# Performance work log

Hardware: AMD Instinct MI355X
Metric: run time of the kernel (lower is better)

The kernel has to match this reference:

```python
import jax, jax.numpy as jnp
import numpy as np

N_NODES = 50000
N_EDGES = 800000
ORIG_FEA = 92
NBR_FEA = 41
HID = 64
N_CONV = 3
BN_EPS = 1e-5


def setup_inputs() -> dict:
    key = jax.random.key(0)
    ks = jax.random.split(key, 16)
    s = 0.05
    inp = {
        "x": jax.random.normal(ks[0], (N_NODES, ORIG_FEA), dtype=jnp.float32),
        "edge_attr": jax.random.normal(ks[1], (N_EDGES, NBR_FEA), dtype=jnp.float32),
        "edge_index": jax.random.randint(ks[2], (2, N_EDGES), 0, N_NODES, dtype=jnp.int64),
        # embedding1 / embedding2
        "W1": jax.random.normal(ks[3], (ORIG_FEA, HID), dtype=jnp.float32) * s,
        "b1": jnp.zeros((HID,), dtype=jnp.float32),
        "W2": jax.random.normal(ks[4], (NBR_FEA, HID), dtype=jnp.float32) * s,
        "b2": jnp.zeros((HID,), dtype=jnp.float32),
        # CGConv lin_f / lin_s per layer, stacked [n_conv, 3*HID, HID]
        "Wf": jax.random.normal(ks[5], (N_CONV, 3 * HID, HID), dtype=jnp.float32) * s,
        "bf": jnp.zeros((N_CONV, HID), dtype=jnp.float32),
        "Ws": jax.random.normal(ks[6], (N_CONV, 3 * HID, HID), dtype=jnp.float32) * s,
        "bs": jnp.zeros((N_CONV, HID), dtype=jnp.float32),
        # BatchNorm1d per layer (training mode: batch statistics)
        "gamma": jnp.ones((N_CONV, HID), dtype=jnp.float32),
        "beta": jnp.zeros((N_CONV, HID), dtype=jnp.float32),
    }
    return inp


def _cgconv(x, e, src, tgt, Wf, bf, Ws, bs):
    # z_ij = [x_i (target), x_j (source), e_ij]  -> [E, 3H]
    z = jnp.concatenate([x[tgt], x[src], e], axis=-1)
    gate = jax.nn.sigmoid(z @ Wf + bf)
    core = jax.nn.softplus(z @ Ws + bs)
    msg = gate * core  # [E, H]
    agg = jax.ops.segment_sum(msg, tgt, num_segments=x.shape[0])
    return x + agg  # residual


def _batchnorm(x, gamma, beta):
    mean = jnp.mean(x, axis=0)
    var = jnp.mean(jnp.square(x - mean), axis=0)  # biased var (torch BN training)
    return (x - mean) * jax.lax.rsqrt(var + BN_EPS) * gamma + beta


def reference(x, edge_attr, edge_index, W1, b1, W2, b2, Wf, bf, Ws, bs, gamma, beta):
    src, tgt = edge_index[0], edge_index[1]
    h = x @ W1 + b1                 # embedding1: [N, H]
    e = edge_attr @ W2 + b2         # embedding2: [E, H]
    for i in range(N_CONV):
        h = _cgconv(h, e, src, tgt, Wf[i], bf[i], Ws[i], bs[i])
        h = _batchnorm(h, gamma[i], beta[i])
        if i < N_CONV - 1:
            h = jax.nn.relu(h)
        # drop_ratio = 0 -> dropout is identity
    return h
```

## Files before the change

kernel.cpp:

```cpp
#include <hip/hip_runtime.h>
#include <cmath>

#define NNODES 50000
#define NEDGES 800000
#define ORIG_FEA 92
#define NBR_FEA 41
#define HID 64
#define BN_EPS 1e-5f

typedef __attribute__((ext_vector_type(8))) short short8;
typedef __attribute__((ext_vector_type(4))) float f32x4;
typedef unsigned short ushort;
typedef unsigned int uint;

static __device__ __forceinline__ ushort f2bf(float f) {
    uint u = __float_as_uint(f);
    uint r = u + 0x7fffu + ((u >> 16) & 1u);
    return (ushort)(r >> 16);
}

__global__ void prep(const float* __restrict__ W2, const float* __restrict__ b2,
                     const float* __restrict__ Wf, const float* __restrict__ bf,
                     const float* __restrict__ Ws, const float* __restrict__ bs,
                     ushort* __restrict__ Bpack, ushort* __restrict__ Tpack,
                     float* __restrict__ bcf, float* __restrict__ bcs,
                     float* __restrict__ stats) {
    if (blockIdx.x == 6) {
        for (int i = threadIdx.x; i < 3 * 128; i += blockDim.x) stats[i] = 0.f;
        return;
    }
    int layer = blockIdx.x >> 1;
    int fs = blockIdx.x & 1;
    const float* Wbig = (fs ? Ws : Wf) + layer * 192 * HID;
    const float* We = Wbig + 128 * HID;
    const float* bvec = (fs ? bs : bf) + layer * HID;
    float* bc = (fs ? bcs : bcf) + layer * HID;
    ushort* Bp = Bpack + layer * 16384 + fs * 8192;
    ushort* Tp = Tpack + layer * 8192 + fs * 4096;

    for (int idx = threadIdx.x; idx < 8192; idx += blockDim.x) {
        int j = idx & 7;
        int lane = (idx >> 3) & 63;
        int ck = (idx >> 9) & 3;
        int tt = (idx >> 11) & 3;
        int k = ck * 32 + ((lane >> 4) * 8) + j;
        int col = tt * 16 + (lane & 15);
        float v = 0.f;
        if (k < 64) v = Wbig[(64 + k) * HID + col];
        else if (k < 64 + NBR_FEA) {
            int r = k - 64;
            float a = 0.f;
            for (int m = 0; m < HID; ++m) a += W2[r * HID + m] * We[m * HID + col];
            v = a;
        }
        Bp[(tt * 4 + ck) * 512 + lane * 8 + j] = f2bf(v);
    }
    for (int idx = threadIdx.x; idx < 4096; idx += blockDim.x) {
        int j = idx & 7;
        int lane = (idx >> 3) & 63;
        int ck = (idx >> 9) & 1;
        int t = (idx >> 10) & 3;
        int k = ck * 32 + ((lane >> 4) * 8) + j;
        int col = t * 16 + (lane & 15);
        Tp[(t * 2 + ck) * 512 + lane * 8 + j] = f2bf(Wbig[k * HID + col]);
    }
    for (int c0 = threadIdx.x; c0 < HID; c0 += blockDim.x) {
        float a = bvec[c0];
        for (int m = 0; m < HID; ++m) a += b2[m] * We[m * HID + c0];
        bc[c0] = a;
    }
}

__global__ void k_hist(const int* __restrict__ eidx, int* __restrict__ deg) {
    int e = blockIdx.x * blockDim.x + threadIdx.x;
    if (e < NEDGES) atomicAdd(&deg[eidx[NEDGES + e]], 1);
}

__global__ void k_blocksum(const int* __restrict__ deg, int* __restrict__ bsum) {
    __shared__ int sh[256];
    int i = blockIdx.x * 256 + threadIdx.x;
    sh[threadIdx.x] = (i < NNODES) ? deg[i] : 0;
    __syncthreads();
    for (int s = 128; s > 0; s >>= 1) {
        if (threadIdx.x < s) sh[threadIdx.x] += sh[threadIdx.x + s];
        __syncthreads();
    }
    if (threadIdx.x == 0) bsum[blockIdx.x] = sh[0];
}

__global__ void k_scanbase(const int* __restrict__ bsum, int* __restrict__ bbase,
                           int* __restrict__ rowptr) {
    __shared__ int sh[256];
    int t = threadIdx.x;
    int v = (t < 196) ? bsum[t] : 0;
    sh[t] = v;
    __syncthreads();
    for (int s = 1; s < 256; s <<= 1) {
        int add = (t >= s) ? sh[t - s] : 0;
        __syncthreads();
        sh[t] += add;
        __syncthreads();
    }
    if (t < 196) bbase[t] = sh[t] - v;
    if (t == 0) rowptr[NNODES] = NEDGES;
}

__global__ void k_writerow(const int* __restrict__ deg, const int* __restrict__ bbase,
                           int* __restrict__ rowptr, int* __restrict__ cursor) {
    __shared__ int sh[256];
    int t = threadIdx.x;
    int i = blockIdx.x * 256 + t;
    int v = (i < NNODES) ? deg[i] : 0;
    sh[t] = v;
    __syncthreads();
    for (int s = 1; s < 256; s <<= 1) {
        int add = (t >= s) ? sh[t - s] : 0;
        __syncthreads();
        sh[t] += add;
        __syncthreads();
    }
    if (i < NNODES) {
        int e = bbase[blockIdx.x] + sh[t] - v;
        rowptr[i] = e;
        cursor[i] = e;
    }
}

__global__ void k_scatterA(const int* __restrict__ eidx, int* __restrict__ cursor,
                           int* __restrict__ eorig, int* __restrict__ srcs) {
    int e = blockIdx.x * blockDim.x + threadIdx.x;
    if (e < NEDGES) {
        int tgt = eidx[NEDGES + e];
        int pos = atomicAdd(&cursor[tgt], 1);
        eorig[pos] = e;
        srcs[pos] = eidx[e];
    }
}

__global__ void k_scatterB(const float* __restrict__ ea, const int* __restrict__ eorig,
                           ushort* __restrict__ eab_s) {
    long idx = (long)blockIdx.x * blockDim.x + threadIdx.x;
    if (idx >= (long)NEDGES * 8) return;
    int pos = (int)(idx >> 3);
    int j = (int)(idx & 7);
    int e = eorig[pos];
    uint w[4];
    #pragma unroll
    for (int m = 0; m < 4; ++m) {
        int k0 = j * 8 + m * 2, k1 = k0 + 1;
        uint u0 = (k0 < NBR_FEA) ? (uint)f2bf(ea[(long)e * NBR_FEA + k0]) : 0u;
        uint u1 = (k1 < NBR_FEA) ? (uint)f2bf(ea[(long)e * NBR_FEA + k1]) : 0u;
        w[m] = u0 | (u1 << 16);
    }
    uint4 o; o.x = w[0]; o.y = w[1]; o.z = w[2]; o.w = w[3];
    *(uint4*)(eab_s + (long)pos * 64 + j * 8) = o;
}

__global__ __launch_bounds__(256) void embed(const float* __restrict__ x,
                                             const float* __restrict__ W1,
                                             const float* __restrict__ b1,
                                             float* __restrict__ h,
                                             ushort* __restrict__ h_bf) {
    int lane = threadIdx.x & 63;
    int wid = (blockIdx.x * blockDim.x + threadIdx.x) >> 6;
    int nw = (gridDim.x * blockDim.x) >> 6;
    float b1v = b1[lane];
    for (int n = wid; n < NNODES; n += nw) {
        const float* xr = x + (long)n * ORIG_FEA;
        float xa = xr[lane];
        float xb = (lane < ORIG_FEA - 64) ? xr[64 + lane] : 0.f;
        float a0 = b1v, a1 = 0.f, a2 = 0.f, a3 = 0.f;
        #pragma unroll
        for (int k = 0; k < 64; k += 4) {
            a0 = fmaf(__shfl(xa, k, 64),     W1[k * HID + lane], a0);
            a1 = fmaf(__shfl(xa, k + 1, 64), W1[(k + 1) * HID + lane], a1);
            a2 = fmaf(__shfl(xa, k + 2, 64), W1[(k + 2) * HID + lane], a2);
            a3 = fmaf(__shfl(xa, k + 3, 64), W1[(k + 3) * HID + lane], a3);
        }
        #pragma unroll
        for (int k = 0; k < ORIG_FEA - 64; k += 4) {
            a0 = fmaf(__shfl(xb, k, 64),     W1[(64 + k) * HID + lane], a0);
            a1 = fmaf(__shfl(xb, k + 1, 64), W1[(65 + k) * HID + lane], a1);
            a2 = fmaf(__shfl(xb, k + 2, 64), W1[(66 + k) * HID + lane], a2);
            a3 = fmaf(__shfl(xb, k + 3, 64), W1[(67 + k) * HID + lane], a3);
        }
        float acc = (a0 + a1) + (a2 + a3);
        h[(long)n * HID + lane] = acc;
        h_bf[(long)n * HID + lane] = f2bf(acc);
    }
}

__global__ __launch_bounds__(256) void proj_mfma(
    const ushort* __restrict__ h_bf, const ushort* __restrict__ Tpack_l,
    const float* __restrict__ bcf_l, const float* __restrict__ bcs_l,
    float* __restrict__ Ttgt) {
    int lane = threadIdx.x & 63;
    int cc = lane & 15;
    int g = lane >> 4;
    short8 Bf[4][2], Bs[4][2];
    #pragma unroll
    for (int t = 0; t < 4; ++t)
        #pragma unroll
        for (int ck = 0; ck < 2; ++ck) {
            Bf[t][ck] = *(const short8*)(Tpack_l + (t * 2 + ck) * 512 + lane * 8);
            Bs[t][ck] = *(const short8*)(Tpack_l + 4096 + (t * 2 + ck) * 512 + lane * 8);
        }
    float bfv[4], bsv[4];
    #pragma unroll
    for (int t = 0; t < 4; ++t) {
        bfv[t] = bcf_l[t * 16 + cc];
        bsv[t] = bcs_l[t * 16 + cc];
    }
    int wid = (blockIdx.x * blockDim.x + threadIdx.x) >> 6;
    int nw = (gridDim.x * blockDim.x) >> 6;
    for (int nb = wid; nb < NNODES / 16; nb += nw) {
        long base = (long)nb * 16;
        long row = base + cc;
        short8 A0 = *(const short8*)(h_bf + row * 64 + g * 8);
        short8 A1 = *(const short8*)(h_bf + row * 64 + 32 + g * 8);
        f32x4 accf[4], accs[4];
        f32x4 z4 = {0.f, 0.f, 0.f, 0.f};
        #pragma unroll
        for (int t = 0; t < 4; ++t) {
            accf[t] = __builtin_amdgcn_mfma_f32_16x16x32_bf16(A0, Bf[t][0], z4, 0, 0, 0);
            accs[t] = __builtin_amdgcn_mfma_f32_16x16x32_bf16(A0, Bs[t][0], z4, 0, 0, 0);
        }
        #pragma unroll
        for (int t = 0; t < 4; ++t) {
            accf[t] = __builtin_amdgcn_mfma_f32_16x16x32_bf16(A1, Bf[t][1], accf[t], 0, 0, 0);
            accs[t] = __builtin_amdgcn_mfma_f32_16x16x32_bf16(A1, Bs[t][1], accs[t], 0, 0, 0);
        }
        #pragma unroll
        for (int r = 0; r < 4; ++r) {
            long node = base + g * 4 + r;
            f32x4 vf = {accf[0][r] + bfv[0], accf[1][r] + bfv[1],
                        accf[2][r] + bfv[2], accf[3][r] + bfv[3]};
            f32x4 vs = {accs[0][r] + bsv[0], accs[1][r] + bsv[1],
                        accs[2][r] + bsv[2], accs[3][r] + bsv[3]};
            *(f32x4*)(Ttgt + node * 128 + cc * 4) = vf;
            *(f32x4*)(Ttgt + node * 128 + 64 + cc * 4) = vs;
        }
    }
}

__global__ __launch_bounds__(256, 2) void edge_kernel(
    const ushort* __restrict__ eab_s, const int* __restrict__ srcs,
    const int* __restrict__ rowptr, const ushort* __restrict__ h_bf,
    const float* __restrict__ h, const float* __restrict__ Ttgt,
    const ushort* __restrict__ Bpack, float* __restrict__ agg,
    float* __restrict__ stats) {
    int lane = threadIdx.x & 63;
    int q = lane >> 4;
    int c = lane & 15;
    int wid = (blockIdx.x * blockDim.x + threadIdx.x) >> 6;
    int nw = (gridDim.x * blockDim.x) >> 6;

    short8 B[8][4];
    #pragma unroll
    for (int t = 0; t < 8; ++t)
        #pragma unroll
        for (int ck = 0; ck < 4; ++ck)
            B[t][ck] = *(const short8*)(Bpack + ((t * 4 + ck) * 512 + lane * 8));

    float st1 = 0.f, st2 = 0.f;
    int tn = wid;
    int r0 = 0, r1 = 0, svAll = 0;
    short8 A0, A1, A2, A3;
    if (tn < NNODES) {
        r0 = rowptr[tn]; r1 = rowptr[tn + 1];
        int e = r0 + lane; if (e > NEDGES - 1) e = NEDGES - 1;
        svAll = srcs[e];
        int sv = __shfl(svAll, c, 64);
        int ei = r0 + c; if (ei > NEDGES - 1) ei = NEDGES - 1;
        const short8* hrow = (const short8*)(h_bf + (long)sv * 64);
        const short8* erow = (const short8*)(eab_s + (long)ei * 64);
        A0 = hrow[q]; A1 = hrow[4 + q]; A2 = erow[q]; A3 = erow[4 + q];
    }

    while (tn < NNODES) {
        int tn2 = tn + nw;
        int r0n = 0, r1n = 0;
        if (tn2 < NNODES) { r0n = rowptr[tn2]; r1n = rowptr[tn2 + 1]; }
        f32x4 tf = *(const f32x4*)(Ttgt + (long)tn * 128 + 4 * c);
        f32x4 ts = *(const f32x4*)(Ttgt + (long)tn * 128 + 64 + 4 * c);
        int d = r1 - r0;
        int nch = (d + 15) >> 4;
        float vs0 = 0.f, vs1 = 0.f, vs2 = 0.f, vs3 = 0.f;

        if (nch == 0) {
            int e = r0n + lane; if (e > NEDGES - 1) e = NEDGES - 1;
            svAll = srcs[e];
            int sv = __shfl(svAll, c, 64);
            int ei = r0n + c; if (ei > NEDGES - 1) ei = NEDGES - 1;
            const short8* hrow = (const short8*)(h_bf + (long)sv * 64);
            const short8* erow = (const short8*)(eab_s + (long)ei * 64);
            A0 = hrow[q]; A1 = hrow[4 + q]; A2 = erow[q]; A3 = erow[4 + q];
        } else {
            for (int ci = 0; ci < nch; ++ci) {
                int sv, ei;
                int nidx = ci + 1;
                if (nidx < nch) {
                    if ((nidx & 3) == 0) {
                        int e = r0 + nidx * 16 + lane;
                        if (e > NEDGES - 1) e = NEDGES - 1;
                        svAll = srcs[e];
                    }
                    sv = __shfl(svAll, ((nidx & 3) << 4) + c, 64);
                    ei = r0 + nidx * 16 + c;
                    if (ei > NEDGES - 1) ei = NEDGES - 1;
                } else {
                    int e = r0n + lane; if (e > NEDGES - 1) e = NEDGES - 1;
                    svAll = srcs[e];
                    sv = __shfl(svAll, c, 64);
                    ei = r0n + c; if (ei > NEDGES - 1) ei = NEDGES - 1;
                }
                const short8* hrow = (const short8*)(h_bf + (long)sv * 64);
                const short8* erow = (const short8*)(eab_s + (long)ei * 64);
                short8 N0 = hrow[q], N1 = hrow[4 + q];
                short8 N2 = erow[q], N3 = erow[4 + q];

                f32x4 accf[4], accs[4];
                f32x4 z4 = {0.f, 0.f, 0.f, 0.f};
                #pragma unroll
                for (int t = 0; t < 4; ++t) {
                    accf[t] = __builtin_amdgcn_mfma_f32_16x16x32_bf16(A0, B[t][0], z4, 0, 0, 0);
                    accs[t] = __builtin_amdgcn_mfma_f32_16x16x32_bf16(A0, B[t + 4][0], z4, 0, 0, 0);
                }
                #pragma unroll
                for (int t = 0; t < 4; ++t) {
                    accf[t] = __builtin_amdgcn_mfma_f32_16x16x32_bf16(A1, B[t][1], accf[t], 0, 0, 0);
                    accs[t] = __builtin_amdgcn_mfma_f32_16x16x32_bf16(A1, B[t + 4][1], accs[t], 0, 0, 0);
                }
                #pragma unroll
                for (int t = 0; t < 4; ++t) {
                    accf[t] = __builtin_amdgcn_mfma_f32_16x16x32_bf16(A2, B[t][2], accf[t], 0, 0, 0);
                    accs[t] = __builtin_amdgcn_mfma_f32_16x16x32_bf16(A2, B[t + 4][2], accs[t], 0, 0, 0);
                }
                #pragma unroll
                for (int t = 0; t < 4; ++t) {
                    accf[t] = __builtin_amdgcn_mfma_f32_16x16x32_bf16(A3, B[t][3], accf[t], 0, 0, 0);
                    accs[t] = __builtin_amdgcn_mfma_f32_16x16x32_bf16(A3, B[t + 4][3], accs[t], 0, 0, 0);
                }

                int base = ci * 16 + q * 4;
                #pragma unroll
                for (int r = 0; r < 4; ++r) {
                    bool valid = (base + r) < d;
                    #pragma unroll
                    for (int t = 0; t < 4; ++t) {
                        float f = accf[t][r] + tf[t];
                        float s = accs[t][r] + ts[t];
                        float g = __builtin_amdgcn_rcpf(1.f + __expf(-f));
                        float sp = fmaxf(s, 0.f) + __logf(1.f + __expf(-fabsf(s)));
                        float msg = valid ? g * sp : 0.f;
                        if (t == 0) vs0 += msg;
                        else if (t == 1) vs1 += msg;
                        else if (t == 2) vs2 += msg;
                        else vs3 += msg;
                    }
                }
                A0 = N0; A1 = N1; A2 = N2; A3 = N3;
            }
        }
        vs0 += __shfl_xor(vs0, 16, 64); vs0 += __shfl_xor(vs0, 32, 64);
        vs1 += __shfl_xor(vs1, 16, 64); vs1 += __shfl_xor(vs1, 32, 64);
        vs2 += __shfl_xor(vs2, 16, 64); vs2 += __shfl_xor(vs2, 32, 64);
        vs3 += __shfl_xor(vs3, 16, 64); vs3 += __shfl_xor(vs3, 32, 64);
        float out = (q == 0) ? vs0 : (q == 1) ? vs1 : (q == 2) ? vs2 : vs3;
        agg[(long)tn * 64 + lane] = out;
        float v = h[(long)tn * 64 + lane] + out;
        st1 += v;
        st2 = fmaf(v, v, st2);

        tn = tn2; r0 = r0n; r1 = r1n;
    }

    __shared__ float ls[4][64], lq[4][64];
    int w = threadIdx.x >> 6;
    ls[w][lane] = st1; lq[w][lane] = st2;
    __syncthreads();
    if (threadIdx.x < 64) {
        float t1 = ls[0][lane] + ls[1][lane] + ls[2][lane] + ls[3][lane];
        float t2 = lq[0][lane] + lq[1][lane] + lq[2][lane] + lq[3][lane];
        atomicAdd(&stats[lane], t1);
        atomicAdd(&stats[64 + lane], t2);
    }
}

__global__ __launch_bounds__(256) void bn_apply(
    float* __restrict__ h, const float* __restrict__ agg,
    const float* __restrict__ stats, const float* __restrict__ gamma,
    const float* __restrict__ beta, ushort* __restrict__ h_bf, int relu) {
    int tid = blockIdx.x * blockDim.x + threadIdx.x;
    int nth = gridDim.x * blockDim.x;
    const float invn = 1.f / (float)NNODES;
    int cb = (tid & 15) * 4;
    f32x4 sc, sh;
    #pragma unroll
    for (int j = 0; j < 4; ++j) {
        float m = stats[cb + j] * invn;
        float v = stats[64 + cb + j] * invn - m * m;
        float s = rsqrtf(v + BN_EPS) * gamma[cb + j];
        sc[j] = s;
        sh[j] = beta[cb + j] - m * s;
    }
    for (long i = tid; i < (long)NNODES * 16; i += nth) {
        f32x4 v = ((const f32x4*)h)[i];
        f32x4 a = ((const f32x4*)agg)[i];
        f32x4 y;
        #pragma unroll
        for (int j = 0; j < 4; ++j) {
            float t = (v[j] + a[j]) * sc[j] + sh[j];
            y[j] = relu ? fmaxf(t, 0.f) : t;
        }
        ((f32x4*)h)[i] = y;
        uint lo = (uint)f2bf(y[0]) | ((uint)f2bf(y[1]) << 16);
        uint hi = (uint)f2bf(y[2]) | ((uint)f2bf(y[3]) << 16);
        uint2 o; o.x = lo; o.y = hi;
        *(uint2*)(h_bf + i * 4) = o;
    }
}

extern "C" void kernel_launch(void* const* d_in, const int* in_sizes, int n_in,
                              void* d_out, int out_size, void* d_ws, size_t ws_size,
                              hipStream_t stream) {
    const float* x    = (const float*)d_in[0];
    const float* ea   = (const float*)d_in[1];
    const int*   eidx = (const int*)d_in[2];
    const float* W1   = (const float*)d_in[3];
    const float* b1   = (const float*)d_in[4];
    const float* W2   = (const float*)d_in[5];
    const float* b2   = (const float*)d_in[6];
    const float* Wf   = (const float*)d_in[7];
    const float* bf   = (const float*)d_in[8];
    const float* Ws   = (const float*)d_in[9];
    const float* bs   = (const float*)d_in[10];
    const float* gamma= (const float*)d_in[11];
    const float* beta = (const float*)d_in[12];
    float* h = (float*)d_out;

    char* wb = (char*)d_ws;
    auto align = [&]() { wb = (char*)(((size_t)wb + 255) & ~(size_t)255); };
    ushort* Bpack = (ushort*)wb;  wb += 3 * 8 * 4 * 512 * sizeof(ushort); align();
    ushort* Tpack = (ushort*)wb;  wb += 3 * 2 * 4 * 2 * 512 * sizeof(ushort); align();
    float* bcf   = (float*)wb;    wb += 3 * HID * sizeof(float);
    float* bcs   = (float*)wb;    wb += 3 * HID * sizeof(float);
    float* stats = (float*)wb;    wb += 3 * 2 * HID * sizeof(float); align();
    int* deg     = (int*)wb;      wb += NNODES * sizeof(int);
    int* rowptr  = (int*)wb;      wb += (NNODES + 1) * sizeof(int);
    int* cursor  = (int*)wb;      wb += NNODES * sizeof(int);
    int* bsum    = (int*)wb;      wb += 256 * sizeof(int);
    int* bbase   = (int*)wb;      wb += 256 * sizeof(int); align();
    int* eorig   = (int*)wb;      wb += NEDGES * sizeof(int);
    int* srcs    = (int*)wb;      wb += NEDGES * sizeof(int);
    align();
    float* Ttgt  = (float*)wb;    wb += (size_t)NNODES * 128 * sizeof(float);
    float* agg   = (float*)wb;    wb += (size_t)NNODES * HID * sizeof(float);
    ushort* h_bf = (ushort*)wb;   wb += (size_t)NNODES * HID * sizeof(ushort);
    ushort* eab_s= (ushort*)wb;   wb += (size_t)NEDGES * 64 * sizeof(ushort);

    prep<<<7, 256, 0, stream>>>(W2, b2, Wf, bf, Ws, bs, Bpack, Tpack, bcf, bcs, stats);

    hipMemsetAsync(deg, 0, NNODES * sizeof(int), stream);
    k_hist<<<(NEDGES + 255) / 256, 256, 0, stream>>>(eidx, deg);
    k_blocksum<<<196, 256, 0, stream>>>(deg, bsum);
    k_scanbase<<<1, 256, 0, stream>>>(bsum, bbase, rowptr);
    k_writerow<<<196, 256, 0, stream>>>(deg, bbase, rowptr, cursor);
    k_scatterA<<<(NEDGES + 255) / 256, 256, 0, stream>>>(eidx, cursor, eorig, srcs);
    k_scatterB<<<(NEDGES * 8 + 255) / 256, 256, 0, stream>>>(ea, eorig, eab_s);

    embed<<<2048, 256, 0, stream>>>(x, W1, b1, h, h_bf);
    proj_mfma<<<1024, 256, 0, stream>>>(h_bf, Tpack, bcf, bcs, Ttgt);

    for (int i = 0; i < 3; ++i) {
        edge_kernel<<<2048, 256, 0, stream>>>(eab_s, srcs, rowptr, h_bf, h, Ttgt,
                                              Bpack + i * 16384, agg, stats + i * 128);
        bn_apply<<<2048, 256, 0, stream>>>(h, agg, stats + i * 128, gamma + i * HID,
                                           beta + i * HID, h_bf, (i < 2) ? 1 : 0);
        if (i < 2)
            proj_mfma<<<1024, 256, 0, stream>>>(h_bf, Tpack + (i + 1) * 8192,
                                                bcf + (i + 1) * HID, bcs + (i + 1) * HID,
                                                Ttgt);
    }
}
```

Measured before the change: 853.3 us.

## Fuse BN with next-layer projection, merge embed with edge scatter, shrink edge rows

Several changes land together. BatchNorm+ReLU is fused with the next layer's target projection, so h_bf no longer makes a round trip through memory. The node embedding is merged into the edge-attribute scatter kernel, and that scatter now works per edge through a position array instead of per sorted slot through eorig. Stored edge rows shrink from 64 to 48 bf16 columns, and the padded tail loads are zeroed. The deg memset moves into prep, and s_setprio is added around the MFMA block. Together these aim to cut launch count and memory traffic, with a risk of tiling or layout bugs in the fused code paths.

Result: faster. 832.0 us (-2.5%).

```diff
diff --git a/kernel.cpp b/kernel.cpp
--- a/kernel.cpp
+++ b/kernel.cpp
@@ -7,6 +7,8 @@
 #define NBR_FEA 41
 #define HID 64
 #define BN_EPS 1e-5f
+#define ECOLS 48
+#define EMB_BLOCKS 1024
 
 typedef __attribute__((ext_vector_type(8))) short short8;
 typedef __attribute__((ext_vector_type(4))) float f32x4;
@@ -24,7 +26,12 @@
                      const float* __restrict__ Ws, const float* __restrict__ bs,
                      ushort* __restrict__ Bpack, ushort* __restrict__ Tpack,
                      float* __restrict__ bcf, float* __restrict__ bcs,
-                     float* __restrict__ stats) {
+                     float* __restrict__ stats, int* __restrict__ deg) {
+    if (blockIdx.x >= 7) {
+        int i = (blockIdx.x - 7) * 256 + threadIdx.x;
+        if (i < NNODES) deg[i] = 0;
+        return;
+    }
     if (blockIdx.x == 6) {
         for (int i = threadIdx.x; i < 3 * 128; i += blockDim.x) stats[i] = 0.f;
         return;
@@ -127,23 +134,57 @@
 }
 
 __global__ void k_scatterA(const int* __restrict__ eidx, int* __restrict__ cursor,
-                           int* __restrict__ eorig, int* __restrict__ srcs) {
+                           int* __restrict__ posarr, int* __restrict__ srcs) {
     int e = blockIdx.x * blockDim.x + threadIdx.x;
     if (e < NEDGES) {
         int tgt = eidx[NEDGES + e];
         int pos = atomicAdd(&cursor[tgt], 1);
-        eorig[pos] = e;
+        posarr[e] = pos;
         srcs[pos] = eidx[e];
     }
 }
 
-__global__ void k_scatterB(const float* __restrict__ ea, const int* __restrict__ eorig,
-                           ushort* __restrict__ eab_s) {
-    long idx = (long)blockIdx.x * blockDim.x + threadIdx.x;
-    if (idx >= (long)NEDGES * 8) return;
-    int pos = (int)(idx >> 3);
-    int j = (int)(idx & 7);
-    int e = eorig[pos];
+__global__ __launch_bounds__(256) void scatterB_embed(
+    const float* __restrict__ ea, const int* __restrict__ posarr,
+    ushort* __restrict__ eab_s,
+    const float* __restrict__ x, const float* __restrict__ W1,
+    const float* __restrict__ b1, float* __restrict__ h,
+    ushort* __restrict__ h_bf) {
+    if (blockIdx.x < EMB_BLOCKS) {
+        int lane = threadIdx.x & 63;
+        int wid = (blockIdx.x * blockDim.x + threadIdx.x) >> 6;
+        int nw = (EMB_BLOCKS * 256) >> 6;
+        float b1v = b1[lane];
+        for (int n = wid; n < NNODES; n += nw) {
+            const float* xr = x + (long)n * ORIG_FEA;
+            float xa = xr[lane];
+            float xb = (lane < ORIG_FEA - 64) ? xr[64 + lane] : 0.f;
+            float a0 = b1v, a1 = 0.f, a2 = 0.f, a3 = 0.f;
+            #pragma unroll
+            for (int k = 0; k < 64; k += 4) {
+                a0 = fmaf(__shfl(xa, k, 64),     W1[k * HID + lane], a0);
+                a1 = fmaf(__shfl(xa, k + 1, 64), W1[(k + 1) * HID + lane], a1);
+                a2 = fmaf(__shfl(xa, k + 2, 64), W1[(k + 2) * HID + lane], a2);
+                a3 = fmaf(__shfl(xa, k + 3, 64), W1[(k + 3) * HID + lane], a3);
+            }
+            #pragma unroll
+            for (int k = 0; k < ORIG_FEA - 64; k += 4) {
+                a0 = fmaf(__shfl(xb, k, 64),     W1[(64 + k) * HID + lane], a0);
+                a1 = fmaf(__shfl(xb, k + 1, 64), W1[(65 + k) * HID + lane], a1);
+                a2 = fmaf(__shfl(xb, k + 2, 64), W1[(66 + k) * HID + lane], a2);
+                a3 = fmaf(__shfl(xb, k + 3, 64), W1[(67 + k) * HID + lane], a3);
+            }
+            float acc = (a0 + a1) + (a2 + a3);
+            h[(long)n * HID + lane] = acc;
+            h_bf[(long)n * HID + lane] = f2bf(acc);
+        }
+        return;
+    }
+    long idx = (long)(blockIdx.x - EMB_BLOCKS) * blockDim.x + threadIdx.x;
+    if (idx >= (long)NEDGES * 6) return;
+    int e = (int)(idx / 6);
+    int j = (int)(idx - (long)e * 6);
+    int p = posarr[e];
     uint w[4];
     #pragma unroll
     for (int m = 0; m < 4; ++m) {
@@ -153,41 +194,7 @@
         w[m] = u0 | (u1 << 16);
     }
     uint4 o; o.x = w[0]; o.y = w[1]; o.z = w[2]; o.w = w[3];
-    *(uint4*)(eab_s + (long)pos * 64 + j * 8) = o;
-}
-
-__global__ __launch_bounds__(256) void embed(const float* __restrict__ x,
-                                             const float* __restrict__ W1,
-                                             const float* __restrict__ b1,
-                                             float* __restrict__ h,
-                                             ushort* __restrict__ h_bf) {
-    int lane = threadIdx.x & 63;
-    int wid = (blockIdx.x * blockDim.x + threadIdx.x) >> 6;
-    int nw = (gridDim.x * blockDim.x) >> 6;
-    float b1v = b1[lane];
-    for (int n = wid; n < NNODES; n += nw) {
-        const float* xr = x + (long)n * ORIG_FEA;
-        float xa = xr[lane];
-        float xb = (lane < ORIG_FEA - 64) ? xr[64 + lane] : 0.f;
-        float a0 = b1v, a1 = 0.f, a2 = 0.f, a3 = 0.f;
-        #pragma unroll
-        for (int k = 0; k < 64; k += 4) {
-            a0 = fmaf(__shfl(xa, k, 64),     W1[k * HID + lane], a0);
-            a1 = fmaf(__shfl(xa, k + 1, 64), W1[(k + 1) * HID + lane], a1);
-            a2 = fmaf(__shfl(xa, k + 2, 64), W1[(k + 2) * HID + lane], a2);
-            a3 = fmaf(__shfl(xa, k + 3, 64), W1[(k + 3) * HID + lane], a3);
-        }
-        #pragma unroll
-        for (int k = 0; k < ORIG_FEA - 64; k += 4) {
-            a0 = fmaf(__shfl(xb, k, 64),     W1[(64 + k) * HID + lane], a0);
-            a1 = fmaf(__shfl(xb, k + 1, 64), W1[(65 + k) * HID + lane], a1);
-            a2 = fmaf(__shfl(xb, k + 2, 64), W1[(66 + k) * HID + lane], a2);
-            a3 = fmaf(__shfl(xb, k + 3, 64), W1[(67 + k) * HID + lane], a3);
-        }
-        float acc = (a0 + a1) + (a2 + a3);
-        h[(long)n * HID + lane] = acc;
-        h_bf[(long)n * HID + lane] = f2bf(acc);
-    }
+    *(uint4*)(eab_s + (long)p * ECOLS + j * 8) = o;
 }
 
 __global__ __launch_bounds__(256) void proj_mfma(
@@ -254,6 +261,7 @@
     int c = lane & 15;
     int wid = (blockIdx.x * blockDim.x + threadIdx.x) >> 6;
     int nw = (gridDim.x * blockDim.x) >> 6;
+    const short8 z8 = {0, 0, 0, 0, 0, 0, 0, 0};
 
     short8 B[8][4];
     #pragma unroll
@@ -273,8 +281,11 @@
         int sv = __shfl(svAll, c, 64);
         int ei = r0 + c; if (ei > NEDGES - 1) ei = NEDGES - 1;
         const short8* hrow = (const short8*)(h_bf + (long)sv * 64);
-        const short8* erow = (const short8*)(eab_s + (long)ei * 64);
-        A0 = hrow[q]; A1 = hrow[4 + q]; A2 = erow[q]; A3 = erow[4 + q];
+        const ushort* erow = eab_s + (long)ei * ECOLS;
+        A0 = hrow[q]; A1 = hrow[4 + q];
+        A2 = *(const short8*)(erow + q * 8);
+        A3 = z8;
+        if (q < 2) A3 = *(const short8*)(erow + 32 + q * 8);
     }
 
     while (tn < NNODES) {
@@ -293,8 +304,11 @@
             int sv = __shfl(svAll, c, 64);
             int ei = r0n + c; if (ei > NEDGES - 1) ei = NEDGES - 1;
             const short8* hrow = (const short8*)(h_bf + (long)sv * 64);
-            const short8* erow = (const short8*)(eab_s + (long)ei * 64);
-            A0 = hrow[q]; A1 = hrow[4 + q]; A2 = erow[q]; A3 = erow[4 + q];
+            const ushort* erow = eab_s + (long)ei * ECOLS;
+            A0 = hrow[q]; A1 = hrow[4 + q];
+            A2 = *(const short8*)(erow + q * 8);
+            A3 = z8;
+            if (q < 2) A3 = *(const short8*)(erow + 32 + q * 8);
         } else {
             for (int ci = 0; ci < nch; ++ci) {
                 int sv, ei;
@@ -315,12 +329,15 @@
                     ei = r0n + c; if (ei > NEDGES - 1) ei = NEDGES - 1;
                 }
                 const short8* hrow = (const short8*)(h_bf + (long)sv * 64);
-                const short8* erow = (const short8*)(eab_s + (long)ei * 64);
+                const ushort* erow = eab_s + (long)ei * ECOLS;
                 short8 N0 = hrow[q], N1 = hrow[4 + q];
-                short8 N2 = erow[q], N3 = erow[4 + q];
+                short8 N2 = *(const short8*)(erow + q * 8);
+                short8 N3 = z8;
+                if (q < 2) N3 = *(const short8*)(erow + 32 + q * 8);
 
                 f32x4 accf[4], accs[4];
                 f32x4 z4 = {0.f, 0.f, 0.f, 0.f};
+                __builtin_amdgcn_s_setprio(1);
                 #pragma unroll
                 for (int t = 0; t < 4; ++t) {
                     accf[t] = __builtin_amdgcn_mfma_f32_16x16x32_bf16(A0, B[t][0], z4, 0, 0, 0);
@@ -341,6 +358,7 @@
                     accf[t] = __builtin_amdgcn_mfma_f32_16x16x32_bf16(A3, B[t][3], accf[t], 0, 0, 0);
                     accs[t] = __builtin_amdgcn_mfma_f32_16x16x32_bf16(A3, B[t + 4][3], accs[t], 0, 0, 0);
                 }
+                __builtin_amdgcn_s_setprio(0);
 
                 int base = ci * 16 + q * 4;
                 #pragma unroll
@@ -387,10 +405,107 @@
     }
 }
 
-__global__ __launch_bounds__(256) void bn_apply(
+__global__ __launch_bounds__(256) void bnproj(
     float* __restrict__ h, const float* __restrict__ agg,
     const float* __restrict__ stats, const float* __restrict__ gamma,
-    const float* __restrict__ beta, ushort* __restrict__ h_bf, int relu) {
+    const float* __restrict__ beta, ushort* __restrict__ h_bf,
+    const ushort* __restrict__ Tpack_l, const float* __restrict__ bcf_l,
+    const float* __restrict__ bcs_l, float* __restrict__ Ttgt) {
+    int lane = threadIdx.x & 63;
+    int cc = lane & 15;
+    int g = lane >> 4;
+    short8 Bf[4][2], Bs[4][2];
+    #pragma unroll
+    for (int t = 0; t < 4; ++t)
+        #pragma unroll
+        for (int ck = 0; ck < 2; ++ck) {
+            Bf[t][ck] = *(const short8*)(Tpack_l + (t * 2 + ck) * 512 + lane * 8);
+            Bs[t][ck] = *(const short8*)(Tpack_l + 4096 + (t * 2 + ck) * 512 + lane * 8);
+        }
+    float bfv[4], bsv[4];
+    #pragma unroll
+    for (int t = 0; t < 4; ++t) {
+        bfv[t] = bcf_l[t * 16 + cc];
+        bsv[t] = bcs_l[t * 16 + cc];
+    }
+    const float invn = 1.f / (float)NNODES;
+    float sc[16], sh[16];
+    #pragma unroll
+    for (int m = 0; m < 16; ++m) {
+        int ch = (m < 8) ? (g * 8 + m) : (32 + g * 8 + (m - 8));
+        float mu = stats[ch] * invn;
+        float va = stats[64 + ch] * invn - mu * mu;
+        float s = rsqrtf(va + BN_EPS) * gamma[ch];
+        sc[m] = s;
+        sh[m] = beta[ch] - mu * s;
+    }
+    int wid = (blockIdx.x * blockDim.x + threadIdx.x) >> 6;
+    int nw = (gridDim.x * blockDim.x) >> 6;
+    for (int nb = wid; nb < NNODES / 16; nb += nw) {
+        long base = (long)nb * 16;
+        long row = base + cc;
+        float* hr = h + row * 64;
+        const float* ar = agg + row * 64;
+        float y[16];
+        #pragma unroll
+        for (int half = 0; half < 2; ++half) {
+            int col = half * 32 + g * 8;
+            f32x4 hv0 = *(const f32x4*)(hr + col);
+            f32x4 hv1 = *(const f32x4*)(hr + col + 4);
+            f32x4 av0 = *(const f32x4*)(ar + col);
+            f32x4 av1 = *(const f32x4*)(ar + col + 4);
+            #pragma unroll
+            for (int m = 0; m < 4; ++m) {
+                float t0 = (hv0[m] + av0[m]) * sc[half * 8 + m] + sh[half * 8 + m];
+                float t1 = (hv1[m] + av1[m]) * sc[half * 8 + 4 + m] + sh[half * 8 + 4 + m];
+                y[half * 8 + m] = fmaxf(t0, 0.f);
+                y[half * 8 + 4 + m] = fmaxf(t1, 0.f);
+            }
+        }
+        f32x4 w0 = {y[0], y[1], y[2], y[3]},   w1 = {y[4], y[5], y[6], y[7]};
+        f32x4 w2 = {y[8], y[9], y[10], y[11]}, w3 = {y[12], y[13], y[14], y[15]};
+        *(f32x4*)(hr + g * 8) = w0;       *(f32x4*)(hr + g * 8 + 4) = w1;
+        *(f32x4*)(hr + 32 + g * 8) = w2;  *(f32x4*)(hr + 32 + g * 8 + 4) = w3;
+        uint u[8];
+        #pragma unroll
+        for (int m = 0; m < 8; ++m)
+            u[m] = (uint)f2bf(y[m * 2]) | ((uint)f2bf(y[m * 2 + 1]) << 16);
+        uint4 p0; p0.x = u[0]; p0.y = u[1]; p0.z = u[2]; p0.w = u[3];
+        uint4 p1; p1.x = u[4]; p1.y = u[5]; p1.z = u[6]; p1.w = u[7];
+        *(uint4*)(h_bf + row * 64 + g * 8) = p0;
+        *(uint4*)(h_bf + row * 64 + 32 + g * 8) = p1;
+        short8 A0 = *reinterpret_cast<short8*>(&p0);
+        short8 A1 = *reinterpret_cast<short8*>(&p1);
+
+        f32x4 accf[4], accs[4];
+        f32x4 z4 = {0.f, 0.f, 0.f, 0.f};
+        #pragma unroll
+        for (int t = 0; t < 4; ++t) {
+            accf[t] = __builtin_amdgcn_mfma_f32_16x16x32_bf16(A0, Bf[t][0], z4, 0, 0, 0);
+            accs[t] = __builtin_amdgcn_mfma_f32_16x16x32_bf16(A0, Bs[t][0], z4, 0, 0, 0);
+        }
+        #pragma unroll
+        for (int t = 0; t < 4; ++t) {
+            accf[t] = __builtin_amdgcn_mfma_f32_16x16x32_bf16(A1, Bf[t][1], accf[t], 0, 0, 0);
+            accs[t] = __builtin_amdgcn_mfma_f32_16x16x32_bf16(A1, Bs[t][1], accs[t], 0, 0, 0);
+        }
+        #pragma unroll
+        for (int r = 0; r < 4; ++r) {
+            long node = base + g * 4 + r;
+            f32x4 vf = {accf[0][r] + bfv[0], accf[1][r] + bfv[1],
+                        accf[2][r] + bfv[2], accf[3][r] + bfv[3]};
+            f32x4 vs = {accs[0][r] + bsv[0], accs[1][r] + bsv[1],
+                        accs[2][r] + bsv[2], accs[3][r] + bsv[3]};
+            *(f32x4*)(Ttgt + node * 128 + cc * 4) = vf;
+            *(f32x4*)(Ttgt + node * 128 + 64 + cc * 4) = vs;
+        }
+    }
+}
+
+__global__ __launch_bounds__(256) void bn_final(
+    float* __restrict__ h, const float* __restrict__ agg,
+    const float* __restrict__ stats, const float* __restrict__ gamma,
+    const float* __restrict__ beta) {
     int tid = blockIdx.x * blockDim.x + threadIdx.x;
     int nth = gridDim.x * blockDim.x;
     const float invn = 1.f / (float)NNODES;
@@ -409,15 +524,8 @@
         f32x4 a = ((const f32x4*)agg)[i];
         f32x4 y;
         #pragma unroll
-        for (int j = 0; j < 4; ++j) {
-            float t = (v[j] + a[j]) * sc[j] + sh[j];
-            y[j] = relu ? fmaxf(t, 0.f) : t;
-        }
+        for (int j = 0; j < 4; ++j) y[j] = (v[j] + a[j]) * sc[j] + sh[j];
         ((f32x4*)h)[i] = y;
-        uint lo = (uint)f2bf(y[0]) | ((uint)f2bf(y[1]) << 16);
-        uint hi = (uint)f2bf(y[2]) | ((uint)f2bf(y[3]) << 16);
-        uint2 o; o.x = lo; o.y = hi;
-        *(uint2*)(h_bf + i * 4) = o;
     }
 }
 
@@ -451,35 +559,36 @@
     int* cursor  = (int*)wb;      wb += NNODES * sizeof(int);
     int* bsum    = (int*)wb;      wb += 256 * sizeof(int);
     int* bbase   = (int*)wb;      wb += 256 * sizeof(int); align();
-    int* eorig   = (int*)wb;      wb += NEDGES * sizeof(int);
+    int* posarr  = (int*)wb;      wb += NEDGES * sizeof(int);
     int* srcs    = (int*)wb;      wb += NEDGES * sizeof(int);
     align();
     float* Ttgt  = (float*)wb;    wb += (size_t)NNODES * 128 * sizeof(float);
     float* agg   = (float*)wb;    wb += (size_t)NNODES * HID * sizeof(float);
     ushort* h_bf = (ushort*)wb;   wb += (size_t)NNODES * HID * sizeof(ushort);
-    ushort* eab_s= (ushort*)wb;   wb += (size_t)NEDGES * 64 * sizeof(ushort);
-
-    prep<<<7, 256, 0, stream>>>(W2, b2, Wf, bf, Ws, bs, Bpack, Tpack, bcf, bcs, stats);
-
-    hipMemsetAsync(deg, 0, NNODES * sizeof(int), stream);
+    ushort* eab_s= (ushort*)wb;   wb += (size_t)NEDGES * ECOLS * sizeof(ushort);
+
+    prep<<<203, 256, 0, stream>>>(W2, b2, Wf, bf, Ws, bs, Bpack, Tpack, bcf, bcs,
+                                  stats, deg);
     k_hist<<<(NEDGES + 255) / 256, 256, 0, stream>>>(eidx, deg);
     k_blocksum<<<196, 256, 0, stream>>>(deg, bsum);
     k_scanbase<<<1, 256, 0, stream>>>(bsum, bbase, rowptr);
     k_writerow<<<196, 256, 0, stream>>>(deg, bbase, rowptr, cursor);
-    k_scatterA<<<(NEDGES + 255) / 256, 256, 0, stream>>>(eidx, cursor, eorig, srcs);
-    k_scatterB<<<(NEDGES * 8 + 255) / 256, 256, 0, stream>>>(ea, eorig, eab_s);
-
-    embed<<<2048, 256, 0, stream>>>(x, W1, b1, h, h_bf);
+    k_scatterA<<<(NEDGES + 255) / 256, 256, 0, stream>>>(eidx, cursor, posarr, srcs);
+    scatterB_embed<<<EMB_BLOCKS + (NEDGES * 6 + 255) / 256, 256, 0, stream>>>(
+        ea, posarr, eab_s, x, W1, b1, h, h_bf);
     proj_mfma<<<1024, 256, 0, stream>>>(h_bf, Tpack, bcf, bcs, Ttgt);
 
     for (int i = 0; i < 3; ++i) {
         edge_kernel<<<2048, 256, 0, stream>>>(eab_s, srcs, rowptr, h_bf, h, Ttgt,
                                               Bpack + i * 16384, agg, stats + i * 128);
-        bn_apply<<<2048, 256, 0, stream>>>(h, agg, stats + i * 128, gamma + i * HID,
-                                           beta + i * HID, h_bf, (i < 2) ? 1 : 0);
         if (i < 2)
-            proj_mfma<<<1024, 256, 0, stream>>>(h_bf, Tpack + (i + 1) * 8192,
-                                                bcf + (i + 1) * HID, bcs + (i + 1) * HID,
-                                                Ttgt);
-    }
-}
+            bnproj<<<1024, 256, 0, stream>>>(h, agg, stats + i * 128, gamma + i * HID,
+                                             beta + i * HID, h_bf,
+                                             Tpack + (i + 1) * 8192,
+                                             bcf + (i + 1) * HID, bcs + (i + 1) * HID,
+                                             Ttgt);
+        else
+            bn_final<<<2048, 256, 0, stream>>>(h, agg, stats + i * 128,
+                                               gamma + i * HID, beta + i * HID);
+    }
+}
```
